# Kernel tuning notes

Measured on AMD Instinct MI355X. Metric: run time of the kernel, lower is better.

Reference implementation:

```python
import jax, jax.numpy as jnp
import numpy as np

EMBED = 512
HEADS = 8
HEAD_DIM = EMBED // HEADS
EPS = 1e-5


def setup_inputs() -> dict:
    key = jax.random.key(0)
    ks = jax.random.split(key, 10)
    s = 1.0 / np.sqrt(EMBED)
    x = jax.random.normal(ks[0], (2, 4096, EMBED), dtype=jnp.float32)
    Wq = jax.random.uniform(ks[1], (EMBED, EMBED), jnp.float32, -s, s)
    bq = jnp.zeros((EMBED,), jnp.float32)
    Wk = jax.random.uniform(ks[2], (EMBED, EMBED), jnp.float32, -s, s)
    bk = jnp.zeros((EMBED,), jnp.float32)
    Wv = jax.random.uniform(ks[3], (EMBED, EMBED), jnp.float32, -s, s)
    bv = jnp.zeros((EMBED,), jnp.float32)
    Wo = jax.random.uniform(ks[4], (EMBED, EMBED), jnp.float32, -s, s)
    bo = jnp.zeros((EMBED,), jnp.float32)
    gamma = jnp.ones((EMBED,), jnp.float32)
    beta = jnp.zeros((EMBED,), jnp.float32)
    return {"x": x, "Wq": Wq, "bq": bq, "Wk": Wk, "bk": bk,
            "Wv": Wv, "bv": bv, "Wo": Wo, "bo": bo,
            "gamma": gamma, "beta": beta}


def reference(x, Wq, bq, Wk, bk, Wv, bv, Wo, bo, gamma, beta):
    b, n, e = x.shape
    def split_heads(t):  # [b,n,e] -> [b,h,n,d]
        return t.reshape(b, n, HEADS, HEAD_DIM).transpose(0, 2, 1, 3)
    q = split_heads(x @ Wq + bq)
    k = split_heads(x @ Wk + bk)
    v = split_heads(x @ Wv + bv)
    energy = jnp.einsum('bhqd,bhkd->bhqk', q, k) * (HEAD_DIM ** -0.5)
    attn = jax.nn.softmax(energy, axis=-1)  # dropout=0.0 (eval)
    out = jnp.einsum('bhqk,bhkd->bhqd', attn, v)
    out = out.transpose(0, 2, 1, 3).reshape(b, n, e)
    out = out @ Wo + bo
    y = x + out
    mu = jnp.mean(y, axis=-1, keepdims=True)
    var = jnp.var(y, axis=-1, keepdims=True)
    return (y - mu) * jax.lax.rsqrt(var + EPS) * gamma + beta
```

## Files before the change

### kernel.cpp

```cpp
#include <hip/hip_runtime.h>
#include <hip/hip_bf16.h>


#define ROWS 8192
#define EMB  512
#define SEQ  4096
#define HEADS 8
#define HD   64
#define SPLIT 2
#define QSCALE 0.18033688011112042f

typedef __attribute__((ext_vector_type(8))) short bf16x8;
typedef __attribute__((ext_vector_type(4))) short bf16x4;
typedef __attribute__((ext_vector_type(4))) float f32x4;

#define MFMA_K16(A, B, C) __builtin_amdgcn_mfma_f32_16x16x16bf16_1k(A, B, C, 0, 0, 0)

__device__ __forceinline__ float bf16_to_f(unsigned short u) {
    union { unsigned int i; float f; } v; v.i = ((unsigned int)u) << 16; return v.f;
}
__device__ __forceinline__ unsigned short f_to_bf16(float f) {
    union { __hip_bfloat16 h; unsigned short u; } v; v.h = __float2bfloat16(f); return v.u;
}
__device__ __forceinline__ unsigned int pack_bf16_trunc(float a, float b) {
    return (__float_as_uint(a) >> 16) | (__float_as_uint(b) & 0xFFFF0000u);
}
__device__ __forceinline__ void load_lds16(const void* g, void* l) {
    __builtin_amdgcn_global_load_lds(
        (const __attribute__((address_space(1))) void*)g,
        (__attribute__((address_space(3))) void*)l, 16, 0, 0);
}

__global__ void detect_kernel(const void* x, int* flag) {
    const unsigned short* p = (const unsigned short*)x;
    int t = threadIdx.x;
    int cnt = 0;
    for (int i = 0; i < 4; ++i) {
        unsigned short u = p[t * 4 + i];
        int e = (u >> 7) & 0xFF;
        if (e >= 140) cnt++;
    }
    for (int off = 32; off > 0; off >>= 1) cnt += __shfl_down(cnt, off, 64);
    if (t == 0) *flag = (cnt > 16) ? 1 : 0;
}

__global__ __launch_bounds__(256) void conv_x_kernel(const void* __restrict__ x,
        float* __restrict__ xf, unsigned short* __restrict__ xb, const int* __restrict__ flag) {
    if (*flag == 0) return;
    int i = (blockIdx.x * 256 + threadIdx.x) * 4;
    float4 v = *(const float4*)((const float*)x + i);
    *(float4*)(xf + i) = v;
    ushort4 u = { f_to_bf16(v.x), f_to_bf16(v.y), f_to_bf16(v.z), f_to_bf16(v.w) };
    *(ushort4*)(xb + i) = u;
}

__global__ __launch_bounds__(256) void conv_wt_kernel(
        const void* W0, const void* W1, const void* W2, const void* W3,
        unsigned short* __restrict__ Wt, const int* __restrict__ flag) {
    __shared__ float T[64][65];
    int tid = threadIdx.x;
    int kt = blockIdx.x, nt = blockIdx.y, mat = blockIdx.z;
    const void* src = (mat == 0) ? W0 : (mat == 1) ? W1 : (mat == 2) ? W2 : W3;
    int fp32 = *flag;
    for (int ii = 0; ii < 4; ++ii) {
        int idx = tid + ii * 256;
        int i = idx >> 4, j = (idx & 15) * 4;
        size_t g = (size_t)(kt * 64 + i) * 512 + nt * 64 + j;
        if (fp32) {
            float4 v = *(const float4*)((const float*)src + g);
            T[i][j] = v.x; T[i][j+1] = v.y; T[i][j+2] = v.z; T[i][j+3] = v.w;
        } else {
            ushort4 u = *(const ushort4*)((const unsigned short*)src + g);
            T[i][j] = bf16_to_f(u.x); T[i][j+1] = bf16_to_f(u.y);
            T[i][j+2] = bf16_to_f(u.z); T[i][j+3] = bf16_to_f(u.w);
        }
    }
    __syncthreads();
    for (int ii = 0; ii < 2; ++ii) {
        int idx = tid + ii * 256;
        int j = idx >> 3, ch = idx & 7;
        unsigned short pk[8];
        for (int t = 0; t < 8; ++t) pk[t] = f_to_bf16(T[ch * 8 + t][j]);
        *(bf16x8*)&Wt[(size_t)(mat * 512 + nt * 64 + j) * 512 + kt * 64 + ch * 8] = *(bf16x8*)pk;
    }
}

__global__ __launch_bounds__(256) void conv_small_kernel(
        const void* b0, const void* b1, const void* b2, const void* b3,
        const void* b4, const void* b5, float* __restrict__ dst, const int* __restrict__ flag) {
    int idx = blockIdx.x * 256 + threadIdx.x;
    int mat = idx >> 9, off = idx & 511;
    const void* src = (mat == 0) ? b0 : (mat == 1) ? b1 : (mat == 2) ? b2 :
                      (mat == 3) ? b3 : (mat == 4) ? b4 : b5;
    float v;
    if (*flag) v = ((const float*)src)[off];
    else       v = bf16_to_f(((const unsigned short*)src)[off]);
    dst[idx] = v;
}

template <typename OutT>
__global__ __launch_bounds__(256) void gemm_mfma_kernel(
        const unsigned short* __restrict__ A_conv, const unsigned short* __restrict__ A_raw,
        const int* __restrict__ flag,
        const unsigned short* __restrict__ Bt,
        const float* __restrict__ bias, OutT* __restrict__ C, int ldc, int scale_cols,
        unsigned short* __restrict__ VtOut) {
    __shared__ unsigned short At[128 * 64];
    __shared__ unsigned short Bs[128 * 64];
    const unsigned short* A = (*flag) ? A_conv : A_raw;
    int tid = threadIdx.x;
    int wave = tid >> 6, lane = tid & 63;
    int l15 = lane & 15, quad = lane >> 4;

    int lin = blockIdx.x + gridDim.x * blockIdx.y;
    int nwg = gridDim.x * gridDim.y;
    int bx, by;
    if (nwg & 7) { bx = blockIdx.x; by = blockIdx.y; }
    else {
        int t = (lin & 7) * (nwg >> 3) + (lin >> 3);
        bx = t % gridDim.x; by = t / gridDim.x;
    }
    int m0 = by * 128, n0 = bx * 128;
    int wm = (wave & 1) * 64, wn = (wave >> 1) * 64;

    int rt = wave * 32 + (lane >> 3);
    int ch = (lane & 7) ^ ((lane >> 3) & 7);
    const unsigned short* ag = A  + (size_t)(m0 + rt) * 512 + ch * 8;
    const unsigned short* bg = Bt + (size_t)(n0 + rt) * 512 + ch * 8;

    f32x4 acc[4][4];
    for (int i = 0; i < 4; ++i) for (int j = 0; j < 4; ++j) acc[i][j] = (f32x4){0.f,0.f,0.f,0.f};

    for (int k0 = 0; k0 < 512; k0 += 64) {
        __syncthreads();
        #pragma unroll
        for (int j = 0; j < 4; ++j) {
            load_lds16(ag + (size_t)(j * 8) * 512 + k0, &At[(wave * 32 + j * 8) * 64]);
            load_lds16(bg + (size_t)(j * 8) * 512 + k0, &Bs[(wave * 32 + j * 8) * 64]);
        }
        __syncthreads();
        #pragma unroll
        for (int ks = 0; ks < 2; ++ks) {
            bf16x8 a[4], b[4];
            #pragma unroll
            for (int f = 0; f < 4; ++f) {
                int pc = ((ks * 4 + quad) ^ (l15 & 7)) * 8;
                a[f] = *(const bf16x8*)&At[(wm + f * 16 + l15) * 64 + pc];
                b[f] = *(const bf16x8*)&Bs[(wn + f * 16 + l15) * 64 + pc];
            }
            #pragma unroll
            for (int fm = 0; fm < 4; ++fm)
                #pragma unroll
                for (int fn = 0; fn < 4; ++fn)
                    acc[fm][fn] = __builtin_amdgcn_mfma_f32_16x16x32_bf16(a[fm], b[fn], acc[fm][fn], 0, 0, 0);
        }
    }
    #pragma unroll
    for (int fm = 0; fm < 4; ++fm) {
        #pragma unroll
        for (int fn = 0; fn < 4; ++fn) {
            int col = n0 + wn + fn * 16 + l15;
            float bia = bias[col];
            float sc = (col < scale_cols) ? QSCALE : 1.f;
            int rowbase = m0 + wm + fm * 16 + quad * 4;
            float v0 = (acc[fm][fn][0] + bia) * sc;
            float v1 = (acc[fm][fn][1] + bia) * sc;
            float v2 = (acc[fm][fn][2] + bia) * sc;
            float v3 = (acc[fm][fn][3] + bia) * sc;
            if (VtOut && col >= 1024) {
                int hd = col - 1024;
                int bh = (rowbase >> 12) * 8 + (hd >> 6);
                int d  = hd & 63;
                ushort4 pk = { f_to_bf16(v0), f_to_bf16(v1), f_to_bf16(v2), f_to_bf16(v3) };
                *(ushort4*)&VtOut[((size_t)(bh * 64 + d)) * SEQ + (rowbase & 4095)] = pk;
            } else {
                if constexpr (sizeof(OutT) == 2) {
                    C[(size_t)(rowbase + 0) * ldc + col] = (OutT)f_to_bf16(v0);
                    C[(size_t)(rowbase + 1) * ldc + col] = (OutT)f_to_bf16(v1);
                    C[(size_t)(rowbase + 2) * ldc + col] = (OutT)f_to_bf16(v2);
                    C[(size_t)(rowbase + 3) * ldc + col] = (OutT)f_to_bf16(v3);
                } else {
                    C[(size_t)(rowbase + 0) * ldc + col] = v0;
                    C[(size_t)(rowbase + 1) * ldc + col] = v1;
                    C[(size_t)(rowbase + 2) * ldc + col] = v2;
                    C[(size_t)(rowbase + 3) * ldc + col] = v3;
                }
            }
        }
    }
}

__global__ __launch_bounds__(256, 4) void attn_kernel(
        const unsigned short* __restrict__ QKV, const unsigned short* __restrict__ Vt,
        float* __restrict__ Opart, float* __restrict__ Lpart) {
    __shared__ __align__(16) unsigned char smem[32768];
    unsigned short* Ks = (unsigned short*)smem;
    unsigned short* Vs = (unsigned short*)(smem + 16384);
    float* Ored = (float*)smem;
    float* Lred = (float*)(smem + 16384);

    int tid = threadIdx.x;
    int wave = tid >> 6, lane = tid & 63;
    int l15 = lane & 15, quad = lane >> 4;
    int qh = wave >> 1, kh = wave & 1;
    int lin = blockIdx.x;
    int xcd = lin & 7, slot = lin >> 3;
    int grp = xcd + 8 * (slot >> 6);
    int qt = slot & 63;
    int h = grp & 7, b = (grp >> 3) & 1, s = grp >> 4;
    int bh = b * HEADS + h;
    int k0base = s * (SEQ / SPLIT);
    size_t qrow0 = (size_t)b * SEQ + qt * 64;

    bf16x8 aq[2][2];
    #pragma unroll
    for (int t = 0; t < 2; ++t) {
        const unsigned short* qp = &QKV[(qrow0 + qh * 32 + t * 16 + l15) * 1536 + h * 64];
        aq[t][0] = *(const bf16x8*)&qp[quad * 8];
        aq[t][1] = *(const bf16x8*)&qp[32 + quad * 8];
    }
    f32x4 o[2][4];
    #pragma unroll
    for (int t = 0; t < 2; ++t)
        #pragma unroll
        for (int db = 0; db < 4; ++db) o[t][db] = (f32x4){0.f, 0.f, 0.f, 0.f};
    float lp[2] = {0.f, 0.f};

    int krt = wave * 32 + (lane >> 3);
    int kch = (lane & 7) ^ ((lane >> 3) & 7);
    const unsigned short* kg =
        &QKV[((size_t)b * SEQ + k0base + krt) * 1536 + 512 + h * 64 + kch * 8];

    for (int kt = 0; kt < SEQ / SPLIT / 128; ++kt) {
        __syncthreads();
        #pragma unroll
        for (int j = 0; j < 4; ++j) {
            load_lds16(kg + (size_t)(kt * 128 + j * 8) * 1536, &Ks[(wave * 32 + j * 8) * 64]);
            int d = wave * 16 + j * 4 + quad;
            int vch = l15 ^ (d & 7);
            load_lds16(&Vt[((size_t)bh * 64 + d) * SEQ + k0base + kt * 128 + vch * 8],
                       &Vs[(wave * 16 + j * 4) * 128]);
        }
        __syncthreads();

        #pragma unroll
        for (int nb = 0; nb < 4; ++nb) {
            int kc = kh * 64 + nb * 16;
            int krow = kc + l15;
            int key = krow & 7;
            bf16x8 kA0 = *(const bf16x8*)&Ks[krow * 64 + (quad ^ key) * 8];
            bf16x8 kA1 = *(const bf16x8*)&Ks[krow * 64 + ((4 + quad) ^ key) * 8];
            bf16x4 bv[4];
            #pragma unroll
            for (int db = 0; db < 4; ++db) {
                int d = db * 16 + l15;
                int c16 = (kc >> 3) + (quad >> 1);
                int sub = (quad & 1) * 4;
                bv[db] = *(const bf16x4*)&Vs[d * 128 + ((c16 ^ (d & 7)) * 8) + sub];
            }
            #pragma unroll
            for (int t = 0; t < 2; ++t) {
                f32x4 sv = {0.f, 0.f, 0.f, 0.f};
                sv = __builtin_amdgcn_mfma_f32_16x16x32_bf16(kA0, aq[t][0], sv, 0, 0, 0);
                sv = __builtin_amdgcn_mfma_f32_16x16x32_bf16(kA1, aq[t][1], sv, 0, 0, 0);
                float p0 = __builtin_amdgcn_exp2f(sv[0]);
                float p1 = __builtin_amdgcn_exp2f(sv[1]);
                float p2 = __builtin_amdgcn_exp2f(sv[2]);
                float p3 = __builtin_amdgcn_exp2f(sv[3]);
                lp[t] += (p0 + p1) + (p2 + p3);
                union { unsigned int u[2]; bf16x4 v; } ap;
                ap.u[0] = pack_bf16_trunc(p0, p1);
                ap.u[1] = pack_bf16_trunc(p2, p3);
                #pragma unroll
                for (int db = 0; db < 4; ++db)
                    o[t][db] = MFMA_K16(ap.v, bv[db], o[t][db]);
            }
        }
    }

    __syncthreads();
    #pragma unroll
    for (int t = 0; t < 2; ++t) {
        float v = lp[t];
        v += __shfl_xor(v, 16, 64);
        v += __shfl_xor(v, 32, 64);
        if (quad == 0) Lred[(wave * 2 + t) * 16 + l15] = v;
    }
    __syncthreads();
    float* myO = Ored + wave * (16 * 64);
    #pragma unroll
    for (int t = 0; t < 2; ++t) {
        #pragma unroll
        for (int db = 0; db < 4; ++db)
            #pragma unroll
            for (int r = 0; r < 4; ++r)
                myO[(quad * 4 + r) * 64 + db * 16 + l15] = o[t][db][r];
        __syncthreads();
        {
            int q_l = tid >> 3;
            int dg = tid & 7;
            int qh2 = q_l >> 4, qq = q_l & 15;
            const float* r0 = Ored + (qh2 * 2 + 0) * (16 * 64) + qq * 64 + dg * 8;
            const float* r1 = Ored + (qh2 * 2 + 1) * (16 * 64) + qq * 64 + dg * 8;
            float4 a0 = *(const float4*)&r0[0];
            float4 a1 = *(const float4*)&r0[4];
            float4 c0 = *(const float4*)&r1[0];
            float4 c1 = *(const float4*)&r1[4];
            float4 o0 = { a0.x + c0.x, a0.y + c0.y, a0.z + c0.z, a0.w + c0.w };
            float4 o1 = { a1.x + c1.x, a1.y + c1.y, a1.z + c1.z, a1.w + c1.w };
            size_t row = qrow0 + qh2 * 32 + t * 16 + qq;
            float* dst = &Opart[((size_t)s * ROWS + row) * EMB + h * 64 + dg * 8];
            *(float4*)&dst[0] = o0;
            *(float4*)&dst[4] = o1;
            if (dg == 0) {
                float lt = Lred[((qh2 * 2 + 0) * 2 + t) * 16 + qq] +
                           Lred[((qh2 * 2 + 1) * 2 + t) * 16 + qq];
                Lpart[((size_t)s * ROWS + row) * 8 + h] = lt;
            }
        }
        __syncthreads();
    }
}

__global__ __launch_bounds__(256) void merge_kernel(
        const float* __restrict__ Opart, const float* __restrict__ Lpart,
        unsigned short* __restrict__ Ab) {
    int idx4 = (blockIdx.x * 256 + threadIdx.x) * 4;
    int row = idx4 >> 9;
    int h = (idx4 & 511) >> 6;
    float l = 0.f;
    float acc[4] = {0.f, 0.f, 0.f, 0.f};
    #pragma unroll
    for (int s = 0; s < SPLIT; ++s) {
        l += Lpart[((size_t)s * ROWS + row) * 8 + h];
        float4 u = *(const float4*)&Opart[(size_t)s * ROWS * EMB + idx4];
        acc[0] += u.x; acc[1] += u.y; acc[2] += u.z; acc[3] += u.w;
    }
    float inv = 1.f / l;
    ushort4 out = { f_to_bf16(acc[0] * inv), f_to_bf16(acc[1] * inv),
                    f_to_bf16(acc[2] * inv), f_to_bf16(acc[3] * inv) };
    *(ushort4*)&Ab[idx4] = out;
}

__global__ __launch_bounds__(256) void ln_kernel(
        const float* __restrict__ xf, const unsigned short* __restrict__ xraw,
        const unsigned short* __restrict__ P,
        const float* __restrict__ gamma, const float* __restrict__ beta,
        void* __restrict__ out, const int* __restrict__ flag) {
    int row = blockIdx.x * 4 + (threadIdx.x >> 6);
    int t = threadIdx.x & 63;
    int fp32 = *flag;
    float v[8];
    float s = 0.f, ss = 0.f;
    const unsigned short* pp = &P[(size_t)row * EMB + t * 8];
    ushort4 p0 = *(const ushort4*)&pp[0];
    ushort4 p1 = *(const ushort4*)&pp[4];
    float pv[8] = { bf16_to_f(p0.x), bf16_to_f(p0.y), bf16_to_f(p0.z), bf16_to_f(p0.w),
                    bf16_to_f(p1.x), bf16_to_f(p1.y), bf16_to_f(p1.z), bf16_to_f(p1.w) };
    if (fp32) {
        const float* xp = &xf[(size_t)row * EMB + t * 8];
        for (int i = 0; i < 8; i += 4) {
            float4 x4 = *(const float4*)&xp[i];
            v[i] = x4.x + pv[i]; v[i+1] = x4.y + pv[i+1];
            v[i+2] = x4.z + pv[i+2]; v[i+3] = x4.w + pv[i+3];
        }
    } else {
        const unsigned short* xp = &xraw[(size_t)row * EMB + t * 8];
        ushort4 x0 = *(const ushort4*)&xp[0];
        ushort4 x1 = *(const ushort4*)&xp[4];
        v[0] = bf16_to_f(x0.x) + pv[0]; v[1] = bf16_to_f(x0.y) + pv[1];
        v[2] = bf16_to_f(x0.z) + pv[2]; v[3] = bf16_to_f(x0.w) + pv[3];
        v[4] = bf16_to_f(x1.x) + pv[4]; v[5] = bf16_to_f(x1.y) + pv[5];
        v[6] = bf16_to_f(x1.z) + pv[6]; v[7] = bf16_to_f(x1.w) + pv[7];
    }
    for (int i = 0; i < 8; ++i) { s += v[i]; ss += v[i] * v[i]; }
    for (int off = 32; off > 0; off >>= 1) {
        s  += __shfl_xor(s, off, 64);
        ss += __shfl_xor(ss, off, 64);
    }
    float mu = s * (1.f / 512.f);
    float var = ss * (1.f / 512.f) - mu * mu;
    float rs = rsqrtf(var + 1e-5f);
    for (int i = 0; i < 8; ++i) {
        int col = t * 8 + i;
        float y = (v[i] - mu) * rs * gamma[col] + beta[col];
        if (fp32) ((float*)out)[(size_t)row * EMB + col] = y;
        else      ((__hip_bfloat16*)out)[(size_t)row * EMB + col] = __float2bfloat16(y);
    }
}

extern "C" void kernel_launch(void* const* d_in, const int* in_sizes, int n_in,
                              void* d_out, int out_size, void* d_ws, size_t ws_size,
                              hipStream_t stream) {
    char* ws = (char*)d_ws;
    int* flag = (int*)ws;
    char* p = ws + 256;
    float* x_f  = (float*)p;           p += (size_t)ROWS * EMB * 4;
    float* bias_all = (float*)p;       p += 6 * 512 * 4;
    unsigned short* Wt   = (unsigned short*)p; p += (size_t)2048 * 512 * 2;
    unsigned short* QKVb = (unsigned short*)p; p += (size_t)ROWS * 1536 * 2;
    unsigned short* Vt   = (unsigned short*)p; p += (size_t)16 * HD * SEQ * 2;
    unsigned short* xb = (unsigned short*)p;
    unsigned short* Ab = (unsigned short*)p;   p += (size_t)ROWS * EMB * 2;
    float* Opart = (float*)p;
    unsigned short* Pb = (unsigned short*)p;   p += (size_t)SPLIT * ROWS * EMB * 4;
    float* Lpart = (float*)p;          p += (size_t)SPLIT * ROWS * 8 * 4;

    detect_kernel<<<1, 64, 0, stream>>>(d_in[0], flag);

    conv_x_kernel<<<ROWS * EMB / 1024, 256, 0, stream>>>(d_in[0], x_f, xb, flag);
    conv_wt_kernel<<<dim3(8, 8, 4), 256, 0, stream>>>(d_in[1], d_in[3], d_in[5], d_in[7], Wt, flag);
    conv_small_kernel<<<12, 256, 0, stream>>>(d_in[2], d_in[4], d_in[6], d_in[8], d_in[9], d_in[10],
                                              bias_all, flag);

    gemm_mfma_kernel<unsigned short><<<dim3(12, 64), 256, 0, stream>>>(
        xb, (const unsigned short*)d_in[0], flag, Wt, bias_all, QKVb, 1536, 512, Vt);

    attn_kernel<<<dim3(64 * HEADS * 2 * SPLIT), 256, 0, stream>>>(QKVb, Vt, Opart, Lpart);

    merge_kernel<<<ROWS * EMB / 1024, 256, 0, stream>>>(Opart, Lpart, Ab);

    gemm_mfma_kernel<unsigned short><<<dim3(4, 64), 256, 0, stream>>>(
        Ab, Ab, flag, Wt + (size_t)1536 * 512, bias_all + 1536, Pb, 512, 0,
        (unsigned short*)nullptr);

    ln_kernel<<<ROWS / 4, 256, 0, stream>>>(x_f, (const unsigned short*)d_in[0], Pb,
                                            bias_all + 4 * 512, bias_all + 5 * 512, d_out, flag);
}
```

Measured before the change: 255.0 us.

## Drop key split, double-buffer attention K/V tiles, fold merge into attention epilogue

Removes the two-way key split in attention, so each block walks the full sequence and normalizes its output directly to bf16. This eliminates the fp32 partial outputs and the separate merge kernel. The K/V LDS staging becomes double-buffered 64-key tiles, with the next tile's loads issued after the barrier so they overlap compute. It also stops copying x to an fp32 workspace and has the layernorm read the input directly. The trade-off is half as many attention blocks (1024), which lowers parallelism, and a longer serial loop per block.

```diff
diff --git a/kernel.cpp b/kernel.cpp
--- a/kernel.cpp
+++ b/kernel.cpp
@@ -7,7 +7,6 @@
 #define SEQ  4096
 #define HEADS 8
 #define HD   64
-#define SPLIT 2
 #define QSCALE 0.18033688011112042f
 
 typedef __attribute__((ext_vector_type(8))) short bf16x8;
@@ -45,11 +44,10 @@
 }
 
 __global__ __launch_bounds__(256) void conv_x_kernel(const void* __restrict__ x,
-        float* __restrict__ xf, unsigned short* __restrict__ xb, const int* __restrict__ flag) {
+        unsigned short* __restrict__ xb, const int* __restrict__ flag) {
     if (*flag == 0) return;
     int i = (blockIdx.x * 256 + threadIdx.x) * 4;
     float4 v = *(const float4*)((const float*)x + i);
-    *(float4*)(xf + i) = v;
     ushort4 u = { f_to_bf16(v.x), f_to_bf16(v.y), f_to_bf16(v.z), f_to_bf16(v.w) };
     *(ushort4*)(xb + i) = u;
 }
@@ -192,10 +190,8 @@
 
 __global__ __launch_bounds__(256, 4) void attn_kernel(
         const unsigned short* __restrict__ QKV, const unsigned short* __restrict__ Vt,
-        float* __restrict__ Opart, float* __restrict__ Lpart) {
+        unsigned short* __restrict__ Ab) {
     __shared__ __align__(16) unsigned char smem[32768];
-    unsigned short* Ks = (unsigned short*)smem;
-    unsigned short* Vs = (unsigned short*)(smem + 16384);
     float* Ored = (float*)smem;
     float* Lred = (float*)(smem + 16384);
 
@@ -207,9 +203,8 @@
     int xcd = lin & 7, slot = lin >> 3;
     int grp = xcd + 8 * (slot >> 6);
     int qt = slot & 63;
-    int h = grp & 7, b = (grp >> 3) & 1, s = grp >> 4;
+    int h = grp & 7, b = grp >> 3;
     int bh = b * HEADS + h;
-    int k0base = s * (SEQ / SPLIT);
     size_t qrow0 = (size_t)b * SEQ + qt * 64;
 
     bf16x8 aq[2][2];
@@ -226,37 +221,49 @@
         for (int db = 0; db < 4; ++db) o[t][db] = (f32x4){0.f, 0.f, 0.f, 0.f};
     float lp[2] = {0.f, 0.f};
 
-    int krt = wave * 32 + (lane >> 3);
-    int kch = (lane & 7) ^ ((lane >> 3) & 7);
-    const unsigned short* kg =
-        &QKV[((size_t)b * SEQ + k0base + krt) * 1536 + 512 + h * 64 + kch * 8];
-
-    for (int kt = 0; kt < SEQ / SPLIT / 128; ++kt) {
-        __syncthreads();
-        #pragma unroll
-        for (int j = 0; j < 4; ++j) {
-            load_lds16(kg + (size_t)(kt * 128 + j * 8) * 1536, &Ks[(wave * 32 + j * 8) * 64]);
-            int d = wave * 16 + j * 4 + quad;
-            int vch = l15 ^ (d & 7);
-            load_lds16(&Vt[((size_t)bh * 64 + d) * SEQ + k0base + kt * 128 + vch * 8],
-                       &Vs[(wave * 16 + j * 4) * 128]);
-        }
-        __syncthreads();
-
-        #pragma unroll
-        for (int nb = 0; nb < 4; ++nb) {
-            int kc = kh * 64 + nb * 16;
+    int r8 = lane >> 3;
+    int kch = (lane & 7) ^ (r8 & 7);
+    const unsigned short* kg = &QKV[((size_t)b * SEQ + r8) * 1536 + 512 + h * 64 + kch * 8];
+    const unsigned short* vg = &Vt[((size_t)bh * 64 + wave * 16 + r8) * SEQ + kch * 8];
+
+#define STAGE(buf, kt2) do {                                                          \
+        unsigned short* Ksb = (unsigned short*)(smem + (buf) * 8192);                 \
+        unsigned short* Vsb = (unsigned short*)(smem + 16384 + (buf) * 8192);         \
+        load_lds16(kg + (size_t)((kt2) * 64 + wave * 16) * 1536,                      \
+                   &Ksb[(wave * 16) * 64]);                                           \
+        load_lds16(kg + (size_t)((kt2) * 64 + wave * 16 + 8) * 1536,                  \
+                   &Ksb[(wave * 16 + 8) * 64]);                                       \
+        load_lds16(vg + (size_t)((kt2) * 64), &Vsb[(wave * 16) * 64]);                \
+        load_lds16(vg + (size_t)((kt2) * 64) + (size_t)8 * SEQ,                       \
+                   &Vsb[(wave * 16 + 8) * 64]);                                       \
+    } while (0)
+
+    STAGE(0, 0);
+
+    for (int kt = 0; kt < SEQ / 64; ++kt) {
+        int cur = kt & 1;
+        asm volatile("s_waitcnt vmcnt(0)" ::: "memory");
+        __builtin_amdgcn_sched_barrier(0);
+        asm volatile("s_barrier" ::: "memory");
+        __builtin_amdgcn_sched_barrier(0);
+        if (kt + 1 < SEQ / 64) STAGE(cur ^ 1, kt + 1);
+
+        const unsigned short* Ksc = (const unsigned short*)(smem + cur * 8192);
+        const unsigned short* Vsc = (const unsigned short*)(smem + 16384 + cur * 8192);
+        #pragma unroll
+        for (int nb = 0; nb < 2; ++nb) {
+            int kc = kh * 32 + nb * 16;
             int krow = kc + l15;
             int key = krow & 7;
-            bf16x8 kA0 = *(const bf16x8*)&Ks[krow * 64 + (quad ^ key) * 8];
-            bf16x8 kA1 = *(const bf16x8*)&Ks[krow * 64 + ((4 + quad) ^ key) * 8];
+            bf16x8 kA0 = *(const bf16x8*)&Ksc[krow * 64 + (quad ^ key) * 8];
+            bf16x8 kA1 = *(const bf16x8*)&Ksc[krow * 64 + ((4 + quad) ^ key) * 8];
             bf16x4 bv[4];
             #pragma unroll
             for (int db = 0; db < 4; ++db) {
                 int d = db * 16 + l15;
                 int c16 = (kc >> 3) + (quad >> 1);
                 int sub = (quad & 1) * 4;
-                bv[db] = *(const bf16x4*)&Vs[d * 128 + ((c16 ^ (d & 7)) * 8) + sub];
+                bv[db] = *(const bf16x4*)&Vsc[d * 64 + ((c16 ^ (d & 7)) * 8) + sub];
             }
             #pragma unroll
             for (int t = 0; t < 2; ++t) {
@@ -276,7 +283,9 @@
                     o[t][db] = MFMA_K16(ap.v, bv[db], o[t][db]);
             }
         }
-    }
+        __builtin_amdgcn_sched_barrier(0);
+    }
+#undef STAGE
 
     __syncthreads();
     #pragma unroll
@@ -306,40 +315,20 @@
             float4 a1 = *(const float4*)&r0[4];
             float4 c0 = *(const float4*)&r1[0];
             float4 c1 = *(const float4*)&r1[4];
-            float4 o0 = { a0.x + c0.x, a0.y + c0.y, a0.z + c0.z, a0.w + c0.w };
-            float4 o1 = { a1.x + c1.x, a1.y + c1.y, a1.z + c1.z, a1.w + c1.w };
+            float lt = Lred[((qh2 * 2 + 0) * 2 + t) * 16 + qq] +
+                       Lred[((qh2 * 2 + 1) * 2 + t) * 16 + qq];
+            float inv = 1.f / lt;
             size_t row = qrow0 + qh2 * 32 + t * 16 + qq;
-            float* dst = &Opart[((size_t)s * ROWS + row) * EMB + h * 64 + dg * 8];
-            *(float4*)&dst[0] = o0;
-            *(float4*)&dst[4] = o1;
-            if (dg == 0) {
-                float lt = Lred[((qh2 * 2 + 0) * 2 + t) * 16 + qq] +
-                           Lred[((qh2 * 2 + 1) * 2 + t) * 16 + qq];
-                Lpart[((size_t)s * ROWS + row) * 8 + h] = lt;
-            }
+            unsigned short* dst = &Ab[row * EMB + h * 64 + dg * 8];
+            ushort4 lo = { f_to_bf16((a0.x + c0.x) * inv), f_to_bf16((a0.y + c0.y) * inv),
+                           f_to_bf16((a0.z + c0.z) * inv), f_to_bf16((a0.w + c0.w) * inv) };
+            ushort4 hi = { f_to_bf16((a1.x + c1.x) * inv), f_to_bf16((a1.y + c1.y) * inv),
+                           f_to_bf16((a1.z + c1.z) * inv), f_to_bf16((a1.w + c1.w) * inv) };
+            *(ushort4*)&dst[0] = lo;
+            *(ushort4*)&dst[4] = hi;
         }
         __syncthreads();
     }
-}
-
-__global__ __launch_bounds__(256) void merge_kernel(
-        const float* __restrict__ Opart, const float* __restrict__ Lpart,
-        unsigned short* __restrict__ Ab) {
-    int idx4 = (blockIdx.x * 256 + threadIdx.x) * 4;
-    int row = idx4 >> 9;
-    int h = (idx4 & 511) >> 6;
-    float l = 0.f;
-    float acc[4] = {0.f, 0.f, 0.f, 0.f};
-    #pragma unroll
-    for (int s = 0; s < SPLIT; ++s) {
-        l += Lpart[((size_t)s * ROWS + row) * 8 + h];
-        float4 u = *(const float4*)&Opart[(size_t)s * ROWS * EMB + idx4];
-        acc[0] += u.x; acc[1] += u.y; acc[2] += u.z; acc[3] += u.w;
-    }
-    float inv = 1.f / l;
-    ushort4 out = { f_to_bf16(acc[0] * inv), f_to_bf16(acc[1] * inv),
-                    f_to_bf16(acc[2] * inv), f_to_bf16(acc[3] * inv) };
-    *(ushort4*)&Ab[idx4] = out;
 }
 
 __global__ __launch_bounds__(256) void ln_kernel(
@@ -395,20 +384,17 @@
     char* ws = (char*)d_ws;
     int* flag = (int*)ws;
     char* p = ws + 256;
-    float* x_f  = (float*)p;           p += (size_t)ROWS * EMB * 4;
     float* bias_all = (float*)p;       p += 6 * 512 * 4;
     unsigned short* Wt   = (unsigned short*)p; p += (size_t)2048 * 512 * 2;
     unsigned short* QKVb = (unsigned short*)p; p += (size_t)ROWS * 1536 * 2;
     unsigned short* Vt   = (unsigned short*)p; p += (size_t)16 * HD * SEQ * 2;
     unsigned short* xb = (unsigned short*)p;
     unsigned short* Ab = (unsigned short*)p;   p += (size_t)ROWS * EMB * 2;
-    float* Opart = (float*)p;
-    unsigned short* Pb = (unsigned short*)p;   p += (size_t)SPLIT * ROWS * EMB * 4;
-    float* Lpart = (float*)p;          p += (size_t)SPLIT * ROWS * 8 * 4;
+    unsigned short* Pb = (unsigned short*)p;   p += (size_t)ROWS * EMB * 2;
 
     detect_kernel<<<1, 64, 0, stream>>>(d_in[0], flag);
 
-    conv_x_kernel<<<ROWS * EMB / 1024, 256, 0, stream>>>(d_in[0], x_f, xb, flag);
+    conv_x_kernel<<<ROWS * EMB / 1024, 256, 0, stream>>>(d_in[0], xb, flag);
     conv_wt_kernel<<<dim3(8, 8, 4), 256, 0, stream>>>(d_in[1], d_in[3], d_in[5], d_in[7], Wt, flag);
     conv_small_kernel<<<12, 256, 0, stream>>>(d_in[2], d_in[4], d_in[6], d_in[8], d_in[9], d_in[10],
                                               bias_all, flag);
@@ -416,14 +402,13 @@
     gemm_mfma_kernel<unsigned short><<<dim3(12, 64), 256, 0, stream>>>(
         xb, (const unsigned short*)d_in[0], flag, Wt, bias_all, QKVb, 1536, 512, Vt);
 
-    attn_kernel<<<dim3(64 * HEADS * 2 * SPLIT), 256, 0, stream>>>(QKVb, Vt, Opart, Lpart);
-
-    merge_kernel<<<ROWS * EMB / 1024, 256, 0, stream>>>(Opart, Lpart, Ab);
+    attn_kernel<<<dim3(1024), 256, 0, stream>>>(QKVb, Vt, Ab);
 
     gemm_mfma_kernel<unsigned short><<<dim3(4, 64), 256, 0, stream>>>(
         Ab, Ab, flag, Wt + (size_t)1536 * 512, bias_all + 1536, Pb, 512, 0,
         (unsigned short*)nullptr);
 
-    ln_kernel<<<ROWS / 4, 256, 0, stream>>>(x_f, (const unsigned short*)d_in[0], Pb,
+    ln_kernel<<<ROWS / 4, 256, 0, stream>>>((const float*)d_in[0],
+                                            (const unsigned short*)d_in[0], Pb,
                                             bias_all + 4 * 512, bias_all + 5 * 512, d_out, flag);
 }
```

New measurement: 245.5 us. 1.04x faster.
